# Kernel tuning notes

Hardware: AMD Instinct MI355X
Metric: run time of the kernel (lower is better)

Reference implementation:

```python
import jax, jax.numpy as jnp
import numpy as np

B, T, I, H, E, C = 1024, 512, 128, 64, 128, 100

def _lstm_layer(x, W_ih, W_hh, b_ih, b_hh):
    # x: [B, T, in]; PyTorch gate order: i, f, g, o. Returns full output seq [B,T,H] and (h_T, c_T).
    Hh = W_hh.shape[1]
    xg = jnp.einsum('bti,gi->btg', x, W_ih) + b_ih + b_hh  # [B,T,4H], fold both biases
    xg_t = jnp.swapaxes(xg, 0, 1)  # [T,B,4H]

    def step(carry, xg_step):
        h, c = carry
        gates = xg_step + h @ W_hh.T  # [B,4H]
        i, f, g, o = jnp.split(gates, 4, axis=-1)
        i = jax.nn.sigmoid(i); f = jax.nn.sigmoid(f)
        g = jnp.tanh(g);        o = jax.nn.sigmoid(o)
        c = f * c + i * g
        h = o * jnp.tanh(c)
        return (h, c), h

    h0 = jnp.zeros((x.shape[0], Hh), x.dtype)
    (hT, cT), hs = jax.lax.scan(step, (h0, h0), xg_t)
    return jnp.swapaxes(hs, 0, 1), (hT, cT)

def setup_inputs() -> dict:
    key = jax.random.key(0)
    ks = jax.random.split(key, 16)
    s = 1.0 / np.sqrt(H)
    u = lambda k, shp: jax.random.uniform(k, shp, jnp.float32, -s, s)
    return {
        'x': jax.random.normal(ks[0], (B, T, I), jnp.float32),
        'W_ih0': u(ks[1], (4 * H, I)), 'W_hh0': u(ks[2], (4 * H, H)),
        'b_ih0': u(ks[3], (4 * H,)),   'b_hh0': u(ks[4], (4 * H,)),
        'W_ih1': u(ks[5], (4 * H, H)), 'W_hh1': u(ks[6], (4 * H, H)),
        'b_ih1': u(ks[7], (4 * H,)),   'b_hh1': u(ks[8], (4 * H,)),
        'W_proj': u(ks[9], (E, H)),    'b_proj': u(ks[10], (E,)),
        'W_fc1': u(ks[11], (E, E)),    'b_fc1': u(ks[12], (E,)),
        'W_fc2': u(ks[13], (C, E)),    'b_fc2': u(ks[14], (C,)),
    }

def reference(x, W_ih0, W_hh0, b_ih0, b_hh0, W_ih1, W_hh1, b_ih1, b_hh1,
              W_proj, b_proj, W_fc1, b_fc1, W_fc2, b_fc2):
    out1, _ = _lstm_layer(x, W_ih0, W_hh0, b_ih0, b_hh0)      # [B,T,H]
    _, (h_last, _) = _lstm_layer(out1, W_ih1, W_hh1, b_ih1, b_hh1)  # hidden[-1]: [B,H]
    emb = jax.nn.relu(h_last @ W_proj.T + b_proj)             # [B,E]
    hid = jax.nn.relu(emb @ W_fc1.T + b_fc1)                  # dropout = identity (eval)
    return hid @ W_fc2.T + b_fc2                              # [B,C] logits
```

## Files before the change

### kernel.cpp

```cpp
#include <hip/hip_runtime.h>
#include <hip/hip_bf16.h>

#define BB 1024
#define TT 512
#define II 128
#define HH 64
#define G4 256
#define EE 128
#define CC 100
#define NB 4
#define NTH 512

typedef float f2 __attribute__((ext_vector_type(2)));
typedef float f4 __attribute__((ext_vector_type(4)));

__device__ __forceinline__ float sigm(float v) { return 1.f / (1.f + __expf(-v)); }
__device__ __forceinline__ float tanh_f(float v) {
    v = fminf(fmaxf(v, -15.f), 15.f);
    float e = __expf(2.f * v);
    return (e - 1.f) / (e + 1.f);
}

__global__ __launch_bounds__(NTH, 2)
void lstm2_persistent(const float* __restrict__ x,
                      const float* __restrict__ Wih0, const float* __restrict__ Whh0,
                      const float* __restrict__ bih0, const float* __restrict__ bhh0,
                      const float* __restrict__ Wih1, const float* __restrict__ Whh1,
                      const float* __restrict__ bih1, const float* __restrict__ bhh1,
                      float* __restrict__ hlast)
{
    __shared__ float xs[2][NB][II];
    __shared__ float h0s[NB][HH];
    __shared__ float h1s[NB][HH];
    __shared__ float zp0[4][NB][G4];
    __shared__ float zp1[4][NB][G4];
    __shared__ float bs0s[G4], bs1s[G4];

    const int tid = threadIdx.x;
    const int q   = tid >> 7;
    const int r   = tid & 127;
    const int b0  = blockIdx.x * NB;

    f2 w0a[16], w0b[16];
    f2 h0a[8],  h0b[8];
    f2 u1a[8],  u1b[8];
    f2 v1a[8],  v1b[8];

#define LOADW(dst, src, n4)                                          \
    do {                                                             \
        const f4* _s = (const f4*)(src);                             \
        _Pragma("unroll")                                            \
        for (int k = 0; k < (n4); ++k) {                             \
            f4 t = _s[k];                                            \
            dst[2*k]   = (f2){t.x, t.y};                             \
            dst[2*k+1] = (f2){t.z, t.w};                             \
        }                                                            \
    } while (0)

    LOADW(w0a, Wih0 + (size_t)r         * II + q * 32, 8);
    LOADW(w0b, Wih0 + (size_t)(r + 128) * II + q * 32, 8);
    LOADW(h0a, Whh0 + (size_t)r         * HH + q * 16, 4);
    LOADW(h0b, Whh0 + (size_t)(r + 128) * HH + q * 16, 4);
    LOADW(u1a, Wih1 + (size_t)r         * HH + q * 16, 4);
    LOADW(u1b, Wih1 + (size_t)(r + 128) * HH + q * 16, 4);
    LOADW(v1a, Whh1 + (size_t)r         * HH + q * 16, 4);
    LOADW(v1b, Whh1 + (size_t)(r + 128) * HH + q * 16, 4);
#undef LOADW

#define PIN(arr, n)                                                  \
    _Pragma("unroll")                                                \
    for (int _i = 0; _i < (n); ++_i) asm volatile("" : "+v"(arr[_i]))

    if (tid < G4) {
        bs0s[tid] = bih0[tid] + bhh0[tid];
        bs1s[tid] = bih1[tid] + bhh1[tid];
        h0s[tid >> 6][tid & 63] = 0.f;
        h1s[tid >> 6][tid & 63] = 0.f;
    }

    const float* xrow = x + ((size_t)(b0 + q) * TT) * II + r;
    xs[0][q][r] = xrow[0];
    float pre = xrow[II];

    const int cb = (tid >> 6) & 3, cj = tid & 63;
    float c0 = 0.f, c1 = 0.f;

    __syncthreads();

    for (int t = 0; t <= TT; ++t) {
        const int cur = t & 1, nxt = cur ^ 1;

        PIN(w0a, 16); PIN(w0b, 16);
        PIN(h0a, 8);  PIN(h0b, 8);
        PIN(u1a, 8);  PIN(u1b, 8);
        PIN(v1a, 8);  PIN(v1b, 8);

        if (t < TT) {
            f2 aA[NB], aB[NB];
            #pragma unroll
            for (int b = 0; b < NB; ++b) { aA[b] = (f2){0.f, 0.f}; aB[b] = (f2){0.f, 0.f}; }
            #pragma unroll
            for (int b = 0; b < NB; ++b) {
                const f4* xv = (const f4*)&xs[cur][b][q * 32];
                #pragma unroll
                for (int k = 0; k < 8; ++k) {
                    f4 v = xv[k];
                    f2 lo = (f2){v.x, v.y}, hi = (f2){v.z, v.w};
                    aA[b] += w0a[2*k] * lo;  aA[b] += w0a[2*k+1] * hi;
                    aB[b] += w0b[2*k] * lo;  aB[b] += w0b[2*k+1] * hi;
                }
                const f4* hv = (const f4*)&h0s[b][q * 16];
                #pragma unroll
                for (int k = 0; k < 4; ++k) {
                    f4 v = hv[k];
                    f2 lo = (f2){v.x, v.y}, hi = (f2){v.z, v.w};
                    aA[b] += h0a[2*k] * lo;  aA[b] += h0a[2*k+1] * hi;
                    aB[b] += h0b[2*k] * lo;  aB[b] += h0b[2*k+1] * hi;
                }
            }
            #pragma unroll
            for (int b = 0; b < NB; ++b) {
                zp0[q][b][r]       = aA[b].x + aA[b].y;
                zp0[q][b][r + 128] = aB[b].x + aB[b].y;
            }
        }
        if (t >= 1) {
            f2 aA[NB], aB[NB];
            #pragma unroll
            for (int b = 0; b < NB; ++b) { aA[b] = (f2){0.f, 0.f}; aB[b] = (f2){0.f, 0.f}; }
            #pragma unroll
            for (int b = 0; b < NB; ++b) {
                const f4* hv0 = (const f4*)&h0s[b][q * 16];
                #pragma unroll
                for (int k = 0; k < 4; ++k) {
                    f4 v = hv0[k];
                    f2 lo = (f2){v.x, v.y}, hi = (f2){v.z, v.w};
                    aA[b] += u1a[2*k] * lo;  aA[b] += u1a[2*k+1] * hi;
                    aB[b] += u1b[2*k] * lo;  aB[b] += u1b[2*k+1] * hi;
                }
                const f4* hv1 = (const f4*)&h1s[b][q * 16];
                #pragma unroll
                for (int k = 0; k < 4; ++k) {
                    f4 v = hv1[k];
                    f2 lo = (f2){v.x, v.y}, hi = (f2){v.z, v.w};
                    aA[b] += v1a[2*k] * lo;  aA[b] += v1a[2*k+1] * hi;
                    aB[b] += v1b[2*k] * lo;  aB[b] += v1b[2*k+1] * hi;
                }
            }
            #pragma unroll
            for (int b = 0; b < NB; ++b) {
                zp1[q][b][r]       = aA[b].x + aA[b].y;
                zp1[q][b][r + 128] = aB[b].x + aB[b].y;
            }
        }
        if (t < TT - 1) {
            xs[nxt][q][r] = pre;
            int tn = (t + 2 < TT) ? t + 2 : TT - 1;
            pre = xrow[(size_t)tn * II];
        }
        __syncthreads();

        if (tid < G4) {
            if (t < TT) {
                float zi = zp0[0][cb][cj]     + zp0[1][cb][cj]     + zp0[2][cb][cj]     + zp0[3][cb][cj]     + bs0s[cj];
                float zf = zp0[0][cb][64+cj]  + zp0[1][cb][64+cj]  + zp0[2][cb][64+cj]  + zp0[3][cb][64+cj]  + bs0s[64+cj];
                float zg = zp0[0][cb][128+cj] + zp0[1][cb][128+cj] + zp0[2][cb][128+cj] + zp0[3][cb][128+cj] + bs0s[128+cj];
                float zo = zp0[0][cb][192+cj] + zp0[1][cb][192+cj] + zp0[2][cb][192+cj] + zp0[3][cb][192+cj] + bs0s[192+cj];
                float gi = sigm(zi), gf = sigm(zf), gg = tanh_f(zg), go = sigm(zo);
                c0 = gf * c0 + gi * gg;
                h0s[cb][cj] = go * tanh_f(c0);
            }
        } else {
            if (t >= 1) {
                float zi = zp1[0][cb][cj]     + zp1[1][cb][cj]     + zp1[2][cb][cj]     + zp1[3][cb][cj]     + bs1s[cj];
                float zf = zp1[0][cb][64+cj]  + zp1[1][cb][64+cj]  + zp1[2][cb][64+cj]  + zp1[3][cb][64+cj]  + bs1s[64+cj];
                float zg = zp1[0][cb][128+cj] + zp1[1][cb][128+cj] + zp1[2][cb][128+cj] + zp1[3][cb][128+cj] + bs1s[128+cj];
                float zo = zp1[0][cb][192+cj] + zp1[1][cb][192+cj] + zp1[2][cb][192+cj] + zp1[3][cb][192+cj] + bs1s[192+cj];
                float gi = sigm(zi), gf = sigm(zf), gg = tanh_f(zg), go = sigm(zo);
                c1 = gf * c1 + gi * gg;
                h1s[cb][cj] = go * tanh_f(c1);
            }
        }
        __syncthreads();
    }
#undef PIN

    if (tid >= G4) hlast[(size_t)(b0 + cb) * HH + cj] = h1s[cb][cj];
}

__global__ __launch_bounds__(128, 4)
void head_kernel(const float* __restrict__ hlast,
                 const float* __restrict__ Wp, const float* __restrict__ bp,
                 const float* __restrict__ W1, const float* __restrict__ b1,
                 const float* __restrict__ W2, const float* __restrict__ b2,
                 float* __restrict__ out)
{
    __shared__ float hv[HH];
    __shared__ float emb[EE];
    __shared__ float hid[EE];
    const int b = blockIdx.x;
    const int e = threadIdx.x;
    if (e < HH) hv[e] = hlast[(size_t)b * HH + e];
    __syncthreads();
    float z = bp[e];
    #pragma unroll
    for (int j = 0; j < HH; ++j) z += Wp[e * HH + j] * hv[j];
    emb[e] = fmaxf(z, 0.f);
    __syncthreads();
    z = b1[e];
    #pragma unroll
    for (int j = 0; j < EE; ++j) z += W1[e * EE + j] * emb[j];
    hid[e] = fmaxf(z, 0.f);
    __syncthreads();
    if (e < CC) {
        z = b2[e];
        #pragma unroll
        for (int j = 0; j < EE; ++j) z += W2[e * EE + j] * hid[j];
        out[(size_t)b * CC + e] = z;
    }
}

extern "C" void kernel_launch(void* const* d_in, const int* in_sizes, int n_in,
                              void* d_out, int out_size, void* d_ws, size_t ws_size,
                              hipStream_t stream)
{
    const float* x    = (const float*)d_in[0];
    const float* Wih0 = (const float*)d_in[1];
    const float* Whh0 = (const float*)d_in[2];
    const float* bih0 = (const float*)d_in[3];
    const float* bhh0 = (const float*)d_in[4];
    const float* Wih1 = (const float*)d_in[5];
    const float* Whh1 = (const float*)d_in[6];
    const float* bih1 = (const float*)d_in[7];
    const float* bhh1 = (const float*)d_in[8];
    const float* Wp   = (const float*)d_in[9];
    const float* bp   = (const float*)d_in[10];
    const float* W1   = (const float*)d_in[11];
    const float* b1   = (const float*)d_in[12];
    const float* W2   = (const float*)d_in[13];
    const float* b2   = (const float*)d_in[14];

    float* hlast = (float*)d_ws;
    float* out   = (float*)d_out;

    lstm2_persistent<<<BB / NB, NTH, 0, stream>>>(x, Wih0, Whh0, bih0, bhh0,
                                                  Wih1, Whh1, bih1, bhh1, hlast);
    head_kernel<<<BB, EE, 0, stream>>>(hlast, Wp, bp, W1, b1, W2, b2, out);
}
```

Measured before the change: 1.503 ms.

## Double LSTM block threads with 8-way K-split and register-held biases

Grows the persistent LSTM block from 512 to 1024 threads, splitting each gate dot product 8 ways over K instead of 4, so each thread keeps half as many weights in registers and does half the FMAs per step. Per-thread bias sums move from shared memory into registers, and the gate stage is merged into one code path selected by layer index. The aim is shorter per-step latency on the serial recurrence through more parallel work per batch group. The cost is a reduction over 8 partial sums instead of 4, twice the shared memory for partials, and barriers across 16 waves instead of 8, which may lower occupancy.

Measured after the change: 1.562 ms. 4.0% more time.

```diff
diff --git a/kernel.cpp b/kernel.cpp
--- a/kernel.cpp
+++ b/kernel.cpp
@@ -1,5 +1,4 @@
 #include <hip/hip_runtime.h>
-#include <hip/hip_bf16.h>
 
 #define BB 1024
 #define TT 512
@@ -9,7 +8,8 @@
 #define EE 128
 #define CC 100
 #define NB 4
-#define NTH 512
+#define NTH 1024
+#define SK 8
 
 typedef float f2 __attribute__((ext_vector_type(2)));
 typedef float f4 __attribute__((ext_vector_type(4)));
@@ -21,7 +21,7 @@
     return (e - 1.f) / (e + 1.f);
 }
 
-__global__ __launch_bounds__(NTH, 2)
+__global__ __launch_bounds__(NTH, 4)
 void lstm2_persistent(const float* __restrict__ x,
                       const float* __restrict__ Wih0, const float* __restrict__ Whh0,
                       const float* __restrict__ bih0, const float* __restrict__ bhh0,
@@ -32,19 +32,18 @@
     __shared__ float xs[2][NB][II];
     __shared__ float h0s[NB][HH];
     __shared__ float h1s[NB][HH];
-    __shared__ float zp0[4][NB][G4];
-    __shared__ float zp1[4][NB][G4];
-    __shared__ float bs0s[G4], bs1s[G4];
+    __shared__ float zp0[SK][NB][G4];
+    __shared__ float zp1[SK][NB][G4];
 
     const int tid = threadIdx.x;
-    const int q   = tid >> 7;
+    const int e   = tid >> 7;
     const int r   = tid & 127;
     const int b0  = blockIdx.x * NB;
 
-    f2 w0a[16], w0b[16];
-    f2 h0a[8],  h0b[8];
-    f2 u1a[8],  u1b[8];
-    f2 v1a[8],  v1b[8];
+    f2 w0a[8], w0b[8];
+    f2 h0a[4], h0b[4];
+    f2 u1a[4], u1b[4];
+    f2 v1a[4], v1b[4];
 
 #define LOADW(dst, src, n4)                                          \
     do {                                                             \
@@ -57,135 +56,136 @@
         }                                                            \
     } while (0)
 
-    LOADW(w0a, Wih0 + (size_t)r         * II + q * 32, 8);
-    LOADW(w0b, Wih0 + (size_t)(r + 128) * II + q * 32, 8);
-    LOADW(h0a, Whh0 + (size_t)r         * HH + q * 16, 4);
-    LOADW(h0b, Whh0 + (size_t)(r + 128) * HH + q * 16, 4);
-    LOADW(u1a, Wih1 + (size_t)r         * HH + q * 16, 4);
-    LOADW(u1b, Wih1 + (size_t)(r + 128) * HH + q * 16, 4);
-    LOADW(v1a, Whh1 + (size_t)r         * HH + q * 16, 4);
-    LOADW(v1b, Whh1 + (size_t)(r + 128) * HH + q * 16, 4);
+    LOADW(w0a, Wih0 + (size_t)r         * II + e * 16, 4);
+    LOADW(w0b, Wih0 + (size_t)(r + 128) * II + e * 16, 4);
+    LOADW(h0a, Whh0 + (size_t)r         * HH + e * 8, 2);
+    LOADW(h0b, Whh0 + (size_t)(r + 128) * HH + e * 8, 2);
+    LOADW(u1a, Wih1 + (size_t)r         * HH + e * 8, 2);
+    LOADW(u1b, Wih1 + (size_t)(r + 128) * HH + e * 8, 2);
+    LOADW(v1a, Whh1 + (size_t)r         * HH + e * 8, 2);
+    LOADW(v1b, Whh1 + (size_t)(r + 128) * HH + e * 8, 2);
 #undef LOADW
 
 #define PIN(arr, n)                                                  \
     _Pragma("unroll")                                                \
     for (int _i = 0; _i < (n); ++_i) asm volatile("" : "+v"(arr[_i]))
 
-    if (tid < G4) {
-        bs0s[tid] = bih0[tid] + bhh0[tid];
-        bs1s[tid] = bih1[tid] + bhh1[tid];
-        h0s[tid >> 6][tid & 63] = 0.f;
-        h1s[tid >> 6][tid & 63] = 0.f;
-    }
-
-    const float* xrow = x + ((size_t)(b0 + q) * TT) * II + r;
-    xs[0][q][r] = xrow[0];
-    float pre = xrow[II];
-
-    const int cb = (tid >> 6) & 3, cj = tid & 63;
-    float c0 = 0.f, c1 = 0.f;
+    const int lay = tid >> 8;
+    const int cb  = (tid >> 6) & 3, cj = tid & 63;
+    float c_reg = 0.f;
+    float bi_r = 0.f, bf_r = 0.f, bg_r = 0.f, bo_r = 0.f;
+    if (tid < 512) {
+        const float* bih = lay ? bih1 : bih0;
+        const float* bhh = lay ? bhh1 : bhh0;
+        bi_r = bih[cj]       + bhh[cj];
+        bf_r = bih[64 + cj]  + bhh[64 + cj];
+        bg_r = bih[128 + cj] + bhh[128 + cj];
+        bo_r = bih[192 + cj] + bhh[192 + cj];
+    }
+
+    if (tid < 256) {
+        h0s[(tid >> 6) & 3][tid & 63] = 0.f;
+        h1s[(tid >> 6) & 3][tid & 63] = 0.f;
+    }
+
+    const int lrow = (tid >> 7) & 3, lcol = tid & 127;
+    const float* xrow = x + ((size_t)(b0 + lrow) * TT) * II + lcol;
+    float pre = 0.f;
+    if (tid < NB * II) {
+        xs[0][lrow][lcol] = xrow[0];
+        pre = xrow[II];
+    }
 
     __syncthreads();
 
     for (int t = 0; t <= TT; ++t) {
         const int cur = t & 1, nxt = cur ^ 1;
 
-        PIN(w0a, 16); PIN(w0b, 16);
-        PIN(h0a, 8);  PIN(h0b, 8);
-        PIN(u1a, 8);  PIN(u1b, 8);
-        PIN(v1a, 8);  PIN(v1b, 8);
+        PIN(w0a, 8); PIN(w0b, 8);
+        PIN(h0a, 4); PIN(h0b, 4);
+        PIN(u1a, 4); PIN(u1b, 4);
+        PIN(v1a, 4); PIN(v1b, 4);
 
         if (t < TT) {
-            f2 aA[NB], aB[NB];
-            #pragma unroll
-            for (int b = 0; b < NB; ++b) { aA[b] = (f2){0.f, 0.f}; aB[b] = (f2){0.f, 0.f}; }
             #pragma unroll
             for (int b = 0; b < NB; ++b) {
-                const f4* xv = (const f4*)&xs[cur][b][q * 32];
-                #pragma unroll
-                for (int k = 0; k < 8; ++k) {
+                f2 aA = (f2){0.f, 0.f}, aB = (f2){0.f, 0.f};
+                const f4* xv = (const f4*)&xs[cur][b][e * 16];
+                #pragma unroll
+                for (int k = 0; k < 4; ++k) {
                     f4 v = xv[k];
                     f2 lo = (f2){v.x, v.y}, hi = (f2){v.z, v.w};
-                    aA[b] += w0a[2*k] * lo;  aA[b] += w0a[2*k+1] * hi;
-                    aB[b] += w0b[2*k] * lo;  aB[b] += w0b[2*k+1] * hi;
-                }
-                const f4* hv = (const f4*)&h0s[b][q * 16];
-                #pragma unroll
-                for (int k = 0; k < 4; ++k) {
+                    aA += w0a[2*k] * lo;  aA += w0a[2*k+1] * hi;
+                    aB += w0b[2*k] * lo;  aB += w0b[2*k+1] * hi;
+                }
+                const f4* hv = (const f4*)&h0s[b][e * 8];
+                #pragma unroll
+                for (int k = 0; k < 2; ++k) {
                     f4 v = hv[k];
                     f2 lo = (f2){v.x, v.y}, hi = (f2){v.z, v.w};
-                    aA[b] += h0a[2*k] * lo;  aA[b] += h0a[2*k+1] * hi;
-                    aB[b] += h0b[2*k] * lo;  aB[b] += h0b[2*k+1] * hi;
-                }
+                    aA += h0a[2*k] * lo;  aA += h0a[2*k+1] * hi;
+                    aB += h0b[2*k] * lo;  aB += h0b[2*k+1] * hi;
+                }
+                zp0[e][b][r]       = aA.x + aA.y;
+                zp0[e][b][r + 128] = aB.x + aB.y;
             }
+        }
+        if (t >= 1) {
             #pragma unroll
             for (int b = 0; b < NB; ++b) {
-                zp0[q][b][r]       = aA[b].x + aA[b].y;
-                zp0[q][b][r + 128] = aB[b].x + aB[b].y;
+                f2 aA = (f2){0.f, 0.f}, aB = (f2){0.f, 0.f};
+                const f4* hv0 = (const f4*)&h0s[b][e * 8];
+                #pragma unroll
+                for (int k = 0; k < 2; ++k) {
+                    f4 v = hv0[k];
+                    f2 lo = (f2){v.x, v.y}, hi = (f2){v.z, v.w};
+                    aA += u1a[2*k] * lo;  aA += u1a[2*k+1] * hi;
+                    aB += u1b[2*k] * lo;  aB += u1b[2*k+1] * hi;
+                }
+                const f4* hv1 = (const f4*)&h1s[b][e * 8];
+                #pragma unroll
+                for (int k = 0; k < 2; ++k) {
+                    f4 v = hv1[k];
+                    f2 lo = (f2){v.x, v.y}, hi = (f2){v.z, v.w};
+                    aA += v1a[2*k] * lo;  aA += v1a[2*k+1] * hi;
+                    aB += v1b[2*k] * lo;  aB += v1b[2*k+1] * hi;
+                }
+                zp1[e][b][r]       = aA.x + aA.y;
+                zp1[e][b][r + 128] = aB.x + aB.y;
             }
         }
-        if (t >= 1) {
-            f2 aA[NB], aB[NB];
-            #pragma unroll
-            for (int b = 0; b < NB; ++b) { aA[b] = (f2){0.f, 0.f}; aB[b] = (f2){0.f, 0.f}; }
-            #pragma unroll
-            for (int b = 0; b < NB; ++b) {
-                const f4* hv0 = (const f4*)&h0s[b][q * 16];
-                #pragma unroll
-                for (int k = 0; k < 4; ++k) {
-                    f4 v = hv0[k];
-                    f2 lo = (f2){v.x, v.y}, hi = (f2){v.z, v.w};
-                    aA[b] += u1a[2*k] * lo;  aA[b] += u1a[2*k+1] * hi;
-                    aB[b] += u1b[2*k] * lo;  aB[b] += u1b[2*k+1] * hi;
-                }
-                const f4* hv1 = (const f4*)&h1s[b][q * 16];
-                #pragma unroll
-                for (int k = 0; k < 4; ++k) {
-                    f4 v = hv1[k];
-                    f2 lo = (f2){v.x, v.y}, hi = (f2){v.z, v.w};
-                    aA[b] += v1a[2*k] * lo;  aA[b] += v1a[2*k+1] * hi;
-                    aB[b] += v1b[2*k] * lo;  aB[b] += v1b[2*k+1] * hi;
-                }
-            }
-            #pragma unroll
-            for (int b = 0; b < NB; ++b) {
-                zp1[q][b][r]       = aA[b].x + aA[b].y;
-                zp1[q][b][r + 128] = aB[b].x + aB[b].y;
-            }
-        }
-        if (t < TT - 1) {
-            xs[nxt][q][r] = pre;
+        if (t < TT - 1 && tid < NB * II) {
+            xs[nxt][lrow][lcol] = pre;
             int tn = (t + 2 < TT) ? t + 2 : TT - 1;
             pre = xrow[(size_t)tn * II];
         }
         __syncthreads();
 
-        if (tid < G4) {
-            if (t < TT) {
-                float zi = zp0[0][cb][cj]     + zp0[1][cb][cj]     + zp0[2][cb][cj]     + zp0[3][cb][cj]     + bs0s[cj];
-                float zf = zp0[0][cb][64+cj]  + zp0[1][cb][64+cj]  + zp0[2][cb][64+cj]  + zp0[3][cb][64+cj]  + bs0s[64+cj];
-                float zg = zp0[0][cb][128+cj] + zp0[1][cb][128+cj] + zp0[2][cb][128+cj] + zp0[3][cb][128+cj] + bs0s[128+cj];
-                float zo = zp0[0][cb][192+cj] + zp0[1][cb][192+cj] + zp0[2][cb][192+cj] + zp0[3][cb][192+cj] + bs0s[192+cj];
+        if (tid < 512) {
+            const bool act = lay ? (t >= 1) : (t < TT);
+            if (act) {
+                float (*zp)[NB][G4] = lay ? zp1 : zp0;
+                float zi = bi_r, zf = bf_r, zg = bg_r, zo = bo_r;
+                #pragma unroll
+                for (int p = 0; p < SK; ++p) {
+                    zi += zp[p][cb][cj];
+                    zf += zp[p][cb][64 + cj];
+                    zg += zp[p][cb][128 + cj];
+                    zo += zp[p][cb][192 + cj];
+                }
                 float gi = sigm(zi), gf = sigm(zf), gg = tanh_f(zg), go = sigm(zo);
-                c0 = gf * c0 + gi * gg;
-                h0s[cb][cj] = go * tanh_f(c0);
+                c_reg = gf * c_reg + gi * gg;
+                float h = go * tanh_f(c_reg);
+                if (lay == 0) h0s[cb][cj] = h;
+                else          h1s[cb][cj] = h;
             }
-        } else {
-            if (t >= 1) {
-                float zi = zp1[0][cb][cj]     + zp1[1][cb][cj]     + zp1[2][cb][cj]     + zp1[3][cb][cj]     + bs1s[cj];
-                float zf = zp1[0][cb][64+cj]  + zp1[1][cb][64+cj]  + zp1[2][cb][64+cj]  + zp1[3][cb][64+cj]  + bs1s[64+cj];
-                float zg = zp1[0][cb][128+cj] + zp1[1][cb][128+cj] + zp1[2][cb][128+cj] + zp1[3][cb][128+cj] + bs1s[128+cj];
-                float zo = zp1[0][cb][192+cj] + zp1[1][cb][192+cj] + zp1[2][cb][192+cj] + zp1[3][cb][192+cj] + bs1s[192+cj];
-                float gi = sigm(zi), gf = sigm(zf), gg = tanh_f(zg), go = sigm(zo);
-                c1 = gf * c1 + gi * gg;
-                h1s[cb][cj] = go * tanh_f(c1);
-            }
         }
         __syncthreads();
     }
 #undef PIN
 
-    if (tid >= G4) hlast[(size_t)(b0 + cb) * HH + cj] = h1s[cb][cj];
+    if (tid >= 256 && tid < 512)
+        hlast[(size_t)(b0 + cb) * HH + cj] = h1s[cb][cj];
 }
 
 __global__ __launch_bounds__(128, 4)
```

## Reduce LSTM gate partials with wave shuffles and double-buffer hidden state

Applied to the files above, without the earlier changes.

Threads are remapped so each wave owns 8 hidden units, with 8 lanes splitting the K dimension for all four gates of a unit. Partial dot products are reduced with xor shuffles inside the wave instead of through shared-memory scratch, so each lane can compute the gate nonlinearity directly. Hidden states are double-buffered in shared memory, which cuts the per-step barriers from two to one and removes the zp buffers. In exchange, 8 lanes per unit repeat the nonlinearity, the shuffle count grows, and the per-lane gate selection uses branchy selects.

Measured after the change: 2.363 ms. 1.57x slower.

```diff
diff --git a/kernel.cpp b/kernel.cpp
--- a/kernel.cpp
+++ b/kernel.cpp
@@ -1,5 +1,4 @@
 #include <hip/hip_runtime.h>
-#include <hip/hip_bf16.h>
 
 #define BB 1024
 #define TT 512
@@ -30,23 +29,23 @@
                       float* __restrict__ hlast)
 {
     __shared__ float xs[2][NB][II];
-    __shared__ float h0s[NB][HH];
-    __shared__ float h1s[NB][HH];
-    __shared__ float zp0[4][NB][G4];
-    __shared__ float zp1[4][NB][G4];
-    __shared__ float bs0s[G4], bs1s[G4];
+    __shared__ float h0s[2][NB][HH];
+    __shared__ float h1s[2][NB][HH];
 
     const int tid = threadIdx.x;
-    const int q   = tid >> 7;
-    const int r   = tid & 127;
+    const int w   = tid >> 6;
+    const int l   = tid & 63;
+    const int q   = l & 7;
+    const int jj  = l >> 3;
+    const int j   = w * 8 + jj;
     const int b0  = blockIdx.x * NB;
 
-    f2 w0a[16], w0b[16];
-    f2 h0a[8],  h0b[8];
-    f2 u1a[8],  u1b[8];
-    f2 v1a[8],  v1b[8];
-
-#define LOADW(dst, src, n4)                                          \
+    f2 wx[4][8];
+    f2 wh[4][4];
+    f2 wu[4][4];
+    f2 wv[4][4];
+
+#define LOADR(dst, src, n4)                                          \
     do {                                                             \
         const f4* _s = (const f4*)(src);                             \
         _Pragma("unroll")                                            \
@@ -57,135 +56,146 @@
         }                                                            \
     } while (0)
 
-    LOADW(w0a, Wih0 + (size_t)r         * II + q * 32, 8);
-    LOADW(w0b, Wih0 + (size_t)(r + 128) * II + q * 32, 8);
-    LOADW(h0a, Whh0 + (size_t)r         * HH + q * 16, 4);
-    LOADW(h0b, Whh0 + (size_t)(r + 128) * HH + q * 16, 4);
-    LOADW(u1a, Wih1 + (size_t)r         * HH + q * 16, 4);
-    LOADW(u1b, Wih1 + (size_t)(r + 128) * HH + q * 16, 4);
-    LOADW(v1a, Whh1 + (size_t)r         * HH + q * 16, 4);
-    LOADW(v1b, Whh1 + (size_t)(r + 128) * HH + q * 16, 4);
-#undef LOADW
-
-#define PIN(arr, n)                                                  \
-    _Pragma("unroll")                                                \
-    for (int _i = 0; _i < (n); ++_i) asm volatile("" : "+v"(arr[_i]))
-
-    if (tid < G4) {
-        bs0s[tid] = bih0[tid] + bhh0[tid];
-        bs1s[tid] = bih1[tid] + bhh1[tid];
-        h0s[tid >> 6][tid & 63] = 0.f;
-        h1s[tid >> 6][tid & 63] = 0.f;
+    float bz0[4], bz1[4];
+    #pragma unroll
+    for (int g = 0; g < 4; ++g) {
+        const int R = j + 64 * g;
+        LOADR(wx[g], Wih0 + (size_t)R * II + q * 16, 4);
+        LOADR(wh[g], Whh0 + (size_t)R * HH + q * 8, 2);
+        LOADR(wu[g], Wih1 + (size_t)R * HH + q * 8, 2);
+        LOADR(wv[g], Whh1 + (size_t)R * HH + q * 8, 2);
+        bz0[g] = bih0[R] + bhh0[R];
+        bz1[g] = bih1[R] + bhh1[R];
     }
-
-    const float* xrow = x + ((size_t)(b0 + q) * TT) * II + r;
-    xs[0][q][r] = xrow[0];
+#undef LOADR
+
+    ((float*)h0s)[tid] = 0.f;
+    ((float*)h1s)[tid] = 0.f;
+
+    const int brow = tid >> 7, bcol = tid & 127;
+    const float* xrow = x + ((size_t)(b0 + brow) * TT) * II + bcol;
+    xs[0][brow][bcol] = xrow[0];
     float pre = xrow[II];
 
-    const int cb = (tid >> 6) & 3, cj = tid & 63;
-    float c0 = 0.f, c1 = 0.f;
-
-    __syncthreads();
+    float c0 = 0.f, c1 = 0.f, h1v = 0.f;
+
+    __syncthreads();
+
+#define SEL4(arr, g) ((q & 2) ? ((q & 1) ? arr[3][g] : arr[2][g])   \
+                              : ((q & 1) ? arr[1][g] : arr[0][g]))
 
     for (int t = 0; t <= TT; ++t) {
         const int cur = t & 1, nxt = cur ^ 1;
 
-        PIN(w0a, 16); PIN(w0b, 16);
-        PIN(h0a, 8);  PIN(h0b, 8);
-        PIN(u1a, 8);  PIN(u1b, 8);
-        PIN(v1a, 8);  PIN(v1b, 8);
-
         if (t < TT) {
-            f2 aA[NB], aB[NB];
-            #pragma unroll
-            for (int b = 0; b < NB; ++b) { aA[b] = (f2){0.f, 0.f}; aB[b] = (f2){0.f, 0.f}; }
+            float z0[NB][4];
             #pragma unroll
             for (int b = 0; b < NB; ++b) {
-                const f4* xv = (const f4*)&xs[cur][b][q * 32];
-                #pragma unroll
-                for (int k = 0; k < 8; ++k) {
+                f2 a0 = (f2){0.f,0.f}, a1 = (f2){0.f,0.f},
+                   a2 = (f2){0.f,0.f}, a3 = (f2){0.f,0.f};
+                const f4* xv = (const f4*)&xs[cur][b][q * 16];
+                #pragma unroll
+                for (int k = 0; k < 4; ++k) {
                     f4 v = xv[k];
                     f2 lo = (f2){v.x, v.y}, hi = (f2){v.z, v.w};
-                    aA[b] += w0a[2*k] * lo;  aA[b] += w0a[2*k+1] * hi;
-                    aB[b] += w0b[2*k] * lo;  aB[b] += w0b[2*k+1] * hi;
-                }
-                const f4* hv = (const f4*)&h0s[b][q * 16];
-                #pragma unroll
-                for (int k = 0; k < 4; ++k) {
+                    a0 += wx[0][2*k] * lo;  a0 += wx[0][2*k+1] * hi;
+                    a1 += wx[1][2*k] * lo;  a1 += wx[1][2*k+1] * hi;
+                    a2 += wx[2][2*k] * lo;  a2 += wx[2][2*k+1] * hi;
+                    a3 += wx[3][2*k] * lo;  a3 += wx[3][2*k+1] * hi;
+                }
+                const f4* hv = (const f4*)&h0s[cur][b][q * 8];
+                #pragma unroll
+                for (int k = 0; k < 2; ++k) {
                     f4 v = hv[k];
                     f2 lo = (f2){v.x, v.y}, hi = (f2){v.z, v.w};
-                    aA[b] += h0a[2*k] * lo;  aA[b] += h0a[2*k+1] * hi;
-                    aB[b] += h0b[2*k] * lo;  aB[b] += h0b[2*k+1] * hi;
-                }
+                    a0 += wh[0][2*k] * lo;  a0 += wh[0][2*k+1] * hi;
+                    a1 += wh[1][2*k] * lo;  a1 += wh[1][2*k+1] * hi;
+                    a2 += wh[2][2*k] * lo;  a2 += wh[2][2*k+1] * hi;
+                    a3 += wh[3][2*k] * lo;  a3 += wh[3][2*k+1] * hi;
+                }
+                z0[b][0] = a0.x + a0.y;  z0[b][1] = a1.x + a1.y;
+                z0[b][2] = a2.x + a2.y;  z0[b][3] = a3.x + a3.y;
             }
             #pragma unroll
-            for (int b = 0; b < NB; ++b) {
-                zp0[q][b][r]       = aA[b].x + aA[b].y;
-                zp0[q][b][r + 128] = aB[b].x + aB[b].y;
-            }
+            for (int b = 0; b < NB; ++b)
+                #pragma unroll
+                for (int g = 0; g < 4; ++g) {
+                    float v = z0[b][g];
+                    v += __shfl_xor(v, 1);
+                    v += __shfl_xor(v, 2);
+                    v += __shfl_xor(v, 4);
+                    z0[b][g] = v;
+                }
+            float zi = SEL4(z0, 0) + bz0[0];
+            float zf = SEL4(z0, 1) + bz0[1];
+            float zg = SEL4(z0, 2) + bz0[2];
+            float zo = SEL4(z0, 3) + bz0[3];
+            float gi = sigm(zi), gf = sigm(zf), gg = tanh_f(zg), go = sigm(zo);
+            c0 = gf * c0 + gi * gg;
+            float h = go * tanh_f(c0);
+            if (q < 4) h0s[nxt][q][j] = h;
         }
-        if (t >= 1) {
-            f2 aA[NB], aB[NB];
-            #pragma unroll
-            for (int b = 0; b < NB; ++b) { aA[b] = (f2){0.f, 0.f}; aB[b] = (f2){0.f, 0.f}; }
-            #pragma unroll
-            for (int b = 0; b < NB; ++b) {
-                const f4* hv0 = (const f4*)&h0s[b][q * 16];
-                #pragma unroll
-                for (int k = 0; k < 4; ++k) {
-                    f4 v = hv0[k];
-                    f2 lo = (f2){v.x, v.y}, hi = (f2){v.z, v.w};
-                    aA[b] += u1a[2*k] * lo;  aA[b] += u1a[2*k+1] * hi;
-                    aB[b] += u1b[2*k] * lo;  aB[b] += u1b[2*k+1] * hi;
-                }
-                const f4* hv1 = (const f4*)&h1s[b][q * 16];
-                #pragma unroll
-                for (int k = 0; k < 4; ++k) {
-                    f4 v = hv1[k];
-                    f2 lo = (f2){v.x, v.y}, hi = (f2){v.z, v.w};
-                    aA[b] += v1a[2*k] * lo;  aA[b] += v1a[2*k+1] * hi;
-                    aB[b] += v1b[2*k] * lo;  aB[b] += v1b[2*k+1] * hi;
-                }
-            }
-            #pragma unroll
-            for (int b = 0; b < NB; ++b) {
-                zp1[q][b][r]       = aA[b].x + aA[b].y;
-                zp1[q][b][r + 128] = aB[b].x + aB[b].y;
-            }
-        }
+
         if (t < TT - 1) {
-            xs[nxt][q][r] = pre;
+            xs[nxt][brow][bcol] = pre;
             int tn = (t + 2 < TT) ? t + 2 : TT - 1;
             pre = xrow[(size_t)tn * II];
         }
-        __syncthreads();
-
-        if (tid < G4) {
-            if (t < TT) {
-                float zi = zp0[0][cb][cj]     + zp0[1][cb][cj]     + zp0[2][cb][cj]     + zp0[3][cb][cj]     + bs0s[cj];
-                float zf = zp0[0][cb][64+cj]  + zp0[1][cb][64+cj]  + zp0[2][cb][64+cj]  + zp0[3][cb][64+cj]  + bs0s[64+cj];
-                float zg = zp0[0][cb][128+cj] + zp0[1][cb][128+cj] + zp0[2][cb][128+cj] + zp0[3][cb][128+cj] + bs0s[128+cj];
-                float zo = zp0[0][cb][192+cj] + zp0[1][cb][192+cj] + zp0[2][cb][192+cj] + zp0[3][cb][192+cj] + bs0s[192+cj];
-                float gi = sigm(zi), gf = sigm(zf), gg = tanh_f(zg), go = sigm(zo);
-                c0 = gf * c0 + gi * gg;
-                h0s[cb][cj] = go * tanh_f(c0);
+
+        if (t >= 1) {
+            float z1[NB][4];
+            #pragma unroll
+            for (int b = 0; b < NB; ++b) {
+                f2 a0 = (f2){0.f,0.f}, a1 = (f2){0.f,0.f},
+                   a2 = (f2){0.f,0.f}, a3 = (f2){0.f,0.f};
+                const f4* hv0 = (const f4*)&h0s[cur][b][q * 8];
+                #pragma unroll
+                for (int k = 0; k < 2; ++k) {
+                    f4 v = hv0[k];
+                    f2 lo = (f2){v.x, v.y}, hi = (f2){v.z, v.w};
+                    a0 += wu[0][2*k] * lo;  a0 += wu[0][2*k+1] * hi;
+                    a1 += wu[1][2*k] * lo;  a1 += wu[1][2*k+1] * hi;
+                    a2 += wu[2][2*k] * lo;  a2 += wu[2][2*k+1] * hi;
+                    a3 += wu[3][2*k] * lo;  a3 += wu[3][2*k+1] * hi;
+                }
+                const f4* hv1 = (const f4*)&h1s[cur][b][q * 8];
+                #pragma unroll
+                for (int k = 0; k < 2; ++k) {
+                    f4 v = hv1[k];
+                    f2 lo = (f2){v.x, v.y}, hi = (f2){v.z, v.w};
+                    a0 += wv[0][2*k] * lo;  a0 += wv[0][2*k+1] * hi;
+                    a1 += wv[1][2*k] * lo;  a1 += wv[1][2*k+1] * hi;
+                    a2 += wv[2][2*k] * lo;  a2 += wv[2][2*k+1] * hi;
+                    a3 += wv[3][2*k] * lo;  a3 += wv[3][2*k+1] * hi;
+                }
+                z1[b][0] = a0.x + a0.y;  z1[b][1] = a1.x + a1.y;
+                z1[b][2] = a2.x + a2.y;  z1[b][3] = a3.x + a3.y;
             }
-        } else {
-            if (t >= 1) {
-                float zi = zp1[0][cb][cj]     + zp1[1][cb][cj]     + zp1[2][cb][cj]     + zp1[3][cb][cj]     + bs1s[cj];
-                float zf = zp1[0][cb][64+cj]  + zp1[1][cb][64+cj]  + zp1[2][cb][64+cj]  + zp1[3][cb][64+cj]  + bs1s[64+cj];
-                float zg = zp1[0][cb][128+cj] + zp1[1][cb][128+cj] + zp1[2][cb][128+cj] + zp1[3][cb][128+cj] + bs1s[128+cj];
-                float zo = zp1[0][cb][192+cj] + zp1[1][cb][192+cj] + zp1[2][cb][192+cj] + zp1[3][cb][192+cj] + bs1s[192+cj];
-                float gi = sigm(zi), gf = sigm(zf), gg = tanh_f(zg), go = sigm(zo);
-                c1 = gf * c1 + gi * gg;
-                h1s[cb][cj] = go * tanh_f(c1);
-            }
+            #pragma unroll
+            for (int b = 0; b < NB; ++b)
+                #pragma unroll
+                for (int g = 0; g < 4; ++g) {
+                    float v = z1[b][g];
+                    v += __shfl_xor(v, 1);
+                    v += __shfl_xor(v, 2);
+                    v += __shfl_xor(v, 4);
+                    z1[b][g] = v;
+                }
+            float zi = SEL4(z1, 0) + bz1[0];
+            float zf = SEL4(z1, 1) + bz1[1];
+            float zg = SEL4(z1, 2) + bz1[2];
+            float zo = SEL4(z1, 3) + bz1[3];
+            float gi = sigm(zi), gf = sigm(zf), gg = tanh_f(zg), go = sigm(zo);
+            c1 = gf * c1 + gi * gg;
+            h1v = go * tanh_f(c1);
+            if (q < 4) h1s[nxt][q][j] = h1v;
         }
+
         __syncthreads();
     }
-#undef PIN
-
-    if (tid >= G4) hlast[(size_t)(b0 + cb) * HH + cj] = h1s[cb][cj];
+#undef SEL4
+
+    if (q < 4) hlast[(size_t)(b0 + q) * HH + j] = h1v;
 }
 
 __global__ __launch_bounds__(128, 4)
```
